# Kernel tuning notes

Measured on AMD Instinct MI355X. Metric: run time of the kernel, lower is better.

Reference implementation:

```python
import jax, jax.numpy as jnp
import numpy as np

N_NODES = 65536
N_EDGES = 1048576
IN_CH, HID_CH, OUT_CH = 300, 64, 20
DROPOUT_P = 0.5


def setup_inputs() -> dict:
    key = jax.random.key(0)
    ks = jax.random.split(key, 6)
    x = jax.random.normal(ks[0], (N_NODES, IN_CH), dtype=jnp.float32)
    edge_index = jax.random.randint(ks[1], (2, N_EDGES), 0, N_NODES, dtype=jnp.int64)
    edge_weight = jax.random.uniform(ks[2], (N_EDGES,), dtype=jnp.float32)
    # Glorot-ish init for linear weights (PyG lin has no bias; GCNConv adds its own bias)
    W1 = jax.random.normal(ks[3], (IN_CH, HID_CH), dtype=jnp.float32) / np.sqrt(IN_CH)
    b1 = jnp.zeros((HID_CH,), dtype=jnp.float32)
    W2 = jax.random.normal(ks[4], (HID_CH, OUT_CH), dtype=jnp.float32) / np.sqrt(HID_CH)
    b2 = jnp.zeros((OUT_CH,), dtype=jnp.float32)
    return {"x": x, "edge_index": edge_index, "edge_weight": edge_weight,
            "W1": W1, "b1": b1, "W2": W2, "b2": b2}


def _gcn_conv(x, src, dst, edge_weight, W, b, num_nodes):
    # GCNConv with add_self_loops=False, normalize=False:
    #   h = x @ W; out[i] = sum_{e: dst(e)=i} w_e * h[src(e)]; out += b
    h = x @ W                                   # [N, C_out]
    msg = h[src] * edge_weight[:, None]         # [E, C_out]
    agg = jax.ops.segment_sum(msg, dst, num_segments=num_nodes)
    return agg + b


def reference(x, edge_index, edge_weight, W1, b1, W2, b2):
    num_nodes = x.shape[0]
    src, dst = edge_index[0], edge_index[1]
    h = _gcn_conv(x, src, dst, edge_weight, W1, b1, num_nodes)
    h = jax.nn.relu(h)
    # dropout p=0.5, training=True, deterministic fixed key
    keep = jax.random.bernoulli(jax.random.key(42), 1.0 - DROPOUT_P, h.shape)
    h = jnp.where(keep, h / (1.0 - DROPOUT_P), 0.0)
    out = _gcn_conv(h, src, dst, edge_weight, W2, b2, num_nodes)
    return out
```

## Files before the change

kernel.cpp:

```cpp
#include <hip/hip_runtime.h>

#define N_NODES 65536
#define N_EDGES 1048576
#define NB 256
#define CAP 4608
#define EPB_A 4096
#define BLK_A (N_EDGES / EPB_A)
#define EPT_A (EPB_A / 1024)
#define WT_BLK 20
#define GEMM_BLK (N_NODES / 64)

typedef __attribute__((ext_vector_type(8))) short short8v;
typedef __attribute__((ext_vector_type(4))) float float4v;

__device__ __forceinline__ unsigned short f2bf(float f) {
  unsigned u = __float_as_uint(f);
  unsigned r = u + 0x7FFFu + ((u >> 16) & 1u);
  return (unsigned short)(r >> 16);
}
__device__ __forceinline__ float bflo(unsigned u) { return __uint_as_float(u << 16); }
__device__ __forceinline__ float bfhi(unsigned u) { return __uint_as_float(u & 0xFFFF0000u); }

__device__ __forceinline__ bool keep_mask(unsigned idx) {
  const unsigned k0 = 0u, k1 = 42u;
  const unsigned k2 = 0x1BD11BDAu ^ k0 ^ k1;
  unsigned x0 = 0u;
  unsigned x1 = idx;
  x0 += k0; x1 += k1;
#define TF_ROUND(r) { x0 += x1; x1 = (x1 << (r)) | (x1 >> (32 - (r))); x1 ^= x0; }
  TF_ROUND(13) TF_ROUND(15) TF_ROUND(26) TF_ROUND(6)
  x0 += k1; x1 += k2 + 1u;
  TF_ROUND(17) TF_ROUND(29) TF_ROUND(16) TF_ROUND(24)
  x0 += k2; x1 += k0 + 2u;
  TF_ROUND(13) TF_ROUND(15) TF_ROUND(26) TF_ROUND(6)
  x0 += k0; x1 += k1 + 3u;
  TF_ROUND(17) TF_ROUND(29) TF_ROUND(16) TF_ROUND(24)
  x0 += k1; x1 += k2 + 4u;
  TF_ROUND(13) TF_ROUND(15) TF_ROUND(26) TF_ROUND(6)
  x0 += k2; x1 += k0 + 5u;
#undef TF_ROUND
  return ((x0 ^ x1) & 0x80000000u) == 0u;
}

__global__ __launch_bounds__(1024) void binpass2(const int* __restrict__ ei,
                                                 const float* __restrict__ ew,
                                                 const float* __restrict__ W1,
                                                 unsigned* __restrict__ val2,
                                                 unsigned char* __restrict__ key2,
                                                 unsigned* __restrict__ cnt_mat,
                                                 unsigned* __restrict__ lofs_mat,
                                                 unsigned short* __restrict__ Wt) {
  const int b = blockIdx.x;
  const int t = threadIdx.x;
  if (b >= BLK_A) {
    int i = (b - BLK_A) * 1024 + t;
    int ch = i / 320, k = i % 320;
    Wt[i] = f2bf((k < 300) ? W1[k * 64 + ch] : 0.0f);
    return;
  }
  __shared__ unsigned cnt[NB], lofs[NB], lcur[NB];
  __shared__ unsigned stage_val[EPB_A];
  __shared__ unsigned char stage_key[EPB_A];
  const int e0 = b * EPB_A;
  if (t < NB) { cnt[t] = 0u; lcur[t] = 0u; }
  __syncthreads();
  unsigned pv[EPT_A], pb[EPT_A], pk8[EPT_A];
#pragma unroll
  for (int j = 0; j < EPT_A; ++j) {
    int e = e0 + t + j * 1024;
    unsigned s = (unsigned)ei[e];
    unsigned d = (unsigned)ei[N_EDGES + e];
    pv[j]  = s | ((unsigned)f2bf(ew[e]) << 16);
    pb[j]  = d >> 8;
    pk8[j] = d & 255u;
    atomicAdd(&cnt[pb[j]], 1u);
  }
  __syncthreads();
  if (t < NB) lofs[t] = cnt[t];
  __syncthreads();
  for (int d = 1; d < NB; d <<= 1) {
    unsigned u = 0u;
    if (t < NB && t >= d) u = lofs[t - d];
    __syncthreads();
    if (t < NB) lofs[t] += u;
    __syncthreads();
  }
  if (t < NB) {
    lofs[t] -= cnt[t];
    cnt_mat[(unsigned)b * NB + t]  = cnt[t];
    lofs_mat[(unsigned)b * NB + t] = lofs[t];
  }
  __syncthreads();
#pragma unroll
  for (int j = 0; j < EPT_A; ++j) {
    unsigned bk = pb[j];
    unsigned slot = lofs[bk] + atomicAdd(&lcur[bk], 1u);
    stage_val[slot] = pv[j];
    stage_key[slot] = (unsigned char)pk8[j];
  }
  __syncthreads();
  unsigned* dv = val2 + (size_t)b * EPB_A;
  unsigned char* dk = key2 + (size_t)b * EPB_A;
  for (int s = t; s < EPB_A; s += 1024) { dv[s] = stage_val[s]; dk[s] = stage_key[s]; }
}

__device__ __forceinline__ void bucket_body3(unsigned char* raw, int b,
                                             const unsigned* __restrict__ cnt_mat,
                                             const unsigned* __restrict__ lofs_mat,
                                             const unsigned* __restrict__ val2,
                                             const unsigned char* __restrict__ key2,
                                             unsigned* __restrict__ sortedc,
                                             unsigned* __restrict__ offs_p) {
  unsigned char* kLDS   = raw;
  unsigned* scnt_s  = (unsigned*)(raw + 4608);
  unsigned* sbase_s = scnt_s + NB;
  unsigned* mst_s   = sbase_s + NB;
  unsigned* cnt     = mst_s + NB;
  unsigned* cur     = cnt + NB;
  const int t = threadIdx.x;
  const unsigned scnt = cnt_mat[(unsigned)t * NB + b];
  const unsigned sofs = lofs_mat[(unsigned)t * NB + b];
  scnt_s[t]  = scnt;
  sbase_s[t] = (unsigned)t * EPB_A + sofs;
  cnt[t] = 0u;
  cur[t] = scnt;
  __syncthreads();
  for (int d = 1; d < NB; d <<= 1) {
    unsigned u = (t >= d) ? cur[t - d] : 0u;
    __syncthreads();
    cur[t] += u;
    __syncthreads();
  }
  mst_s[t] = cur[t] - scnt;
  __syncthreads();
  const unsigned n_edges = cur[NB - 1];
  const int g = t >> 4, j0 = t & 15;
  for (int seg = g; seg < NB; seg += 16) {
    const unsigned sc = scnt_s[seg];
    const unsigned sb = sbase_s[seg];
    const unsigned ms = mst_s[seg];
    for (unsigned j = (unsigned)j0; j < sc; j += 16)
      kLDS[ms + j] = key2[sb + j];
  }
  __syncthreads();
  for (unsigned i = t; i < n_edges; i += 256)
    atomicAdd(&cnt[kLDS[i]], 1u);
  __syncthreads();
  const unsigned myc = cnt[t];
  cur[t] = myc;
  __syncthreads();
  for (int d = 1; d < NB; d <<= 1) {
    unsigned u = (t >= d) ? cur[t - d] : 0u;
    __syncthreads();
    cur[t] += u;
    __syncthreads();
  }
  const unsigned lo = (unsigned)b * CAP;
  unsigned excl = cur[t] - myc;
  offs_p[b * NB + t] = (lo + excl) | (myc << 21);
  __syncthreads();
  cur[t] = excl;
  __syncthreads();
  for (int seg = g; seg < NB; seg += 16) {
    const unsigned sc = scnt_s[seg];
    const unsigned sb = sbase_s[seg];
    const unsigned ms = mst_s[seg];
    for (unsigned j = (unsigned)j0; j < sc; j += 16) {
      unsigned v = val2[sb + j];
      unsigned k = kLDS[ms + j];
      unsigned p = lo + atomicAdd(&cur[k], 1u);
      sortedc[p] = v;
    }
  }
}

__device__ __forceinline__ void gemm1_body(unsigned char* smraw, int nb,
                                           const float* __restrict__ x,
                                           const unsigned short* __restrict__ Wt,
                                           unsigned short* __restrict__ h1b) {
  unsigned short (*As)[72] = (unsigned short (*)[72])smraw;
  unsigned short (*Bs)[72] = (unsigned short (*)[72])(smraw + 9216);
  const int t = threadIdx.x;
  const int node0 = nb * 64;
  const int wave = t >> 6, lane = t & 63;
  const int quad = lane >> 4, l16 = lane & 15;
  float4v acc[4] = {{0.f,0.f,0.f,0.f},{0.f,0.f,0.f,0.f},{0.f,0.f,0.f,0.f},{0.f,0.f,0.f,0.f}};

  for (int kt = 0; kt < 5; ++kt) {
    const int k0 = kt * 64;
    for (int f = t; f < 1024; f += 256) {
      int node = f >> 4;
      int k = (f & 15) * 4;
      uint2 packed;
      if (k0 + k < 300) {
        float4 v = *(const float4*)(x + (size_t)(node0 + node) * 300 + k0 + k);
        packed.x = (unsigned)f2bf(v.x) | ((unsigned)f2bf(v.y) << 16);
        packed.y = (unsigned)f2bf(v.z) | ((unsigned)f2bf(v.w) << 16);
      } else {
        packed.x = 0u; packed.y = 0u;
      }
      *(uint2*)&As[node][k] = packed;
    }
    for (int f = t; f < 512; f += 256) {
      int ch = f >> 3;
      int kq = f & 7;
      uint4 v = *(const uint4*)(Wt + (size_t)ch * 320 + k0 + kq * 8);
      *(uint4*)&Bs[ch][kq * 8] = v;
    }
    __syncthreads();
    short8v a0 = *(const short8v*)&As[wave * 16 + l16][quad * 8];
    short8v a1 = *(const short8v*)&As[wave * 16 + l16][32 + quad * 8];
#pragma unroll
    for (int nt = 0; nt < 4; ++nt) {
      short8v b0 = *(const short8v*)&Bs[nt * 16 + l16][quad * 8];
      short8v b1 = *(const short8v*)&Bs[nt * 16 + l16][32 + quad * 8];
      acc[nt] = __builtin_amdgcn_mfma_f32_16x16x32_bf16(a0, b0, acc[nt], 0, 0, 0);
      acc[nt] = __builtin_amdgcn_mfma_f32_16x16x32_bf16(a1, b1, acc[nt], 0, 0, 0);
    }
    __syncthreads();
  }
#pragma unroll
  for (int nt = 0; nt < 4; ++nt) {
#pragma unroll
    for (int r = 0; r < 4; ++r) {
      h1b[(size_t)(node0 + wave * 16 + quad * 4 + r) * 64 + nt * 16 + l16] = f2bf(acc[nt][r]);
    }
  }
}

__global__ __launch_bounds__(256) void bucketsort_gemm1(const unsigned* __restrict__ cnt_mat,
                                                        const unsigned* __restrict__ lofs_mat,
                                                        const unsigned* __restrict__ val2,
                                                        const unsigned char* __restrict__ key2,
                                                        unsigned* __restrict__ sortedc,
                                                        unsigned* __restrict__ offs_p,
                                                        const float* __restrict__ x,
                                                        const unsigned short* __restrict__ Wt,
                                                        unsigned short* __restrict__ h1b) {
  __shared__ __align__(16) unsigned char sm[18432];
  if (blockIdx.x < NB) {
    bucket_body3(sm, blockIdx.x, cnt_mat, lofs_mat, val2, key2, sortedc, offs_p);
  } else {
    gemm1_body(sm, blockIdx.x - NB, x, Wt, h1b);
  }
}

__global__ __launch_bounds__(256) void agg1_gemm2(const unsigned* __restrict__ offs_p,
                                                  const unsigned* __restrict__ sortedc,
                                                  const unsigned short* __restrict__ h1b,
                                                  const float* __restrict__ b1,
                                                  const float* __restrict__ W2,
                                                  unsigned* __restrict__ g32u) {
  __shared__ float h2[16][68];
  __shared__ float w2t[20][68];
  const int t = threadIdx.x;
  const int node0 = blockIdx.x * 16;
  for (int i = t; i < 20 * 64; i += 256) {
    int row = i >> 6, col = i & 63;
    w2t[row][col] = W2[col * 20 + row];
  }
  const int n = t >> 4, cg = t & 15;
  const int node = node0 + n;
  const unsigned op = offs_p[node];
  const unsigned s = op & 0x1FFFFFu;
  const unsigned e_end = s + (op >> 21);
  float4 acc = *(const float4*)(b1 + cg * 4);
  unsigned i = s;
  for (; i + 8 <= e_end; i += 8) {
    unsigned e0 = sortedc[i],     e1 = sortedc[i + 1], e2 = sortedc[i + 2], e3 = sortedc[i + 3];
    unsigned e4 = sortedc[i + 4], e5 = sortedc[i + 5], e6 = sortedc[i + 6], e7 = sortedc[i + 7];
    uint2 v0 = *(const uint2*)(h1b + ((size_t)(e0 & 0xFFFFu)) * 64 + cg * 4);
    uint2 v1 = *(const uint2*)(h1b + ((size_t)(e1 & 0xFFFFu)) * 64 + cg * 4);
    uint2 v2 = *(const uint2*)(h1b + ((size_t)(e2 & 0xFFFFu)) * 64 + cg * 4);
    uint2 v3 = *(const uint2*)(h1b + ((size_t)(e3 & 0xFFFFu)) * 64 + cg * 4);
    uint2 v4 = *(const uint2*)(h1b + ((size_t)(e4 & 0xFFFFu)) * 64 + cg * 4);
    uint2 v5 = *(const uint2*)(h1b + ((size_t)(e5 & 0xFFFFu)) * 64 + cg * 4);
    uint2 v6 = *(const uint2*)(h1b + ((size_t)(e6 & 0xFFFFu)) * 64 + cg * 4);
    uint2 v7 = *(const uint2*)(h1b + ((size_t)(e7 & 0xFFFFu)) * 64 + cg * 4);
    float w0 = bfhi(e0), w1 = bfhi(e1), w2 = bfhi(e2), w3 = bfhi(e3);
    float w4 = bfhi(e4), w5 = bfhi(e5), w6 = bfhi(e6), w7 = bfhi(e7);
    acc.x = fmaf(w0, bflo(v0.x), acc.x); acc.y = fmaf(w0, bfhi(v0.x), acc.y);
    acc.z = fmaf(w0, bflo(v0.y), acc.z); acc.w = fmaf(w0, bfhi(v0.y), acc.w);
    acc.x = fmaf(w1, bflo(v1.x), acc.x); acc.y = fmaf(w1, bfhi(v1.x), acc.y);
    acc.z = fmaf(w1, bflo(v1.y), acc.z); acc.w = fmaf(w1, bfhi(v1.y), acc.w);
    acc.x = fmaf(w2, bflo(v2.x), acc.x); acc.y = fmaf(w2, bfhi(v2.x), acc.y);
    acc.z = fmaf(w2, bflo(v2.y), acc.z); acc.w = fmaf(w2, bfhi(v2.y), acc.w);
    acc.x = fmaf(w3, bflo(v3.x), acc.x); acc.y = fmaf(w3, bfhi(v3.x), acc.y);
    acc.z = fmaf(w3, bflo(v3.y), acc.z); acc.w = fmaf(w3, bfhi(v3.y), acc.w);
    acc.x = fmaf(w4, bflo(v4.x), acc.x); acc.y = fmaf(w4, bfhi(v4.x), acc.y);
    acc.z = fmaf(w4, bflo(v4.y), acc.z); acc.w = fmaf(w4, bfhi(v4.y), acc.w);
    acc.x = fmaf(w5, bflo(v5.x), acc.x); acc.y = fmaf(w5, bfhi(v5.x), acc.y);
    acc.z = fmaf(w5, bflo(v5.y), acc.z); acc.w = fmaf(w5, bfhi(v5.y), acc.w);
    acc.x = fmaf(w6, bflo(v6.x), acc.x); acc.y = fmaf(w6, bfhi(v6.x), acc.y);
    acc.z = fmaf(w6, bflo(v6.y), acc.z); acc.w = fmaf(w6, bfhi(v6.y), acc.w);
    acc.x = fmaf(w7, bflo(v7.x), acc.x); acc.y = fmaf(w7, bfhi(v7.x), acc.y);
    acc.z = fmaf(w7, bflo(v7.y), acc.z); acc.w = fmaf(w7, bfhi(v7.y), acc.w);
  }
  for (; i < e_end; ++i) {
    unsigned e0 = sortedc[i];
    uint2 v0 = *(const uint2*)(h1b + ((size_t)(e0 & 0xFFFFu)) * 64 + cg * 4);
    float w0 = bfhi(e0);
    acc.x = fmaf(w0, bflo(v0.x), acc.x); acc.y = fmaf(w0, bfhi(v0.x), acc.y);
    acc.z = fmaf(w0, bflo(v0.y), acc.z); acc.w = fmaf(w0, bfhi(v0.y), acc.w);
  }
  const unsigned gi = (unsigned)node * 64u + (unsigned)cg * 4u;
  float r[4] = {acc.x, acc.y, acc.z, acc.w};
#pragma unroll
  for (int j = 0; j < 4; ++j) {
    float v = fmaxf(r[j], 0.0f);
    h2[n][cg * 4 + j] = keep_mask(gi + j) ? v * 2.0f : 0.0f;
  }
  __syncthreads();
  float d0 = 0.0f, d1 = 0.0f;
  if (cg < 10) {
    const int c0 = cg * 2, c1 = cg * 2 + 1;
#pragma unroll
    for (int k = 0; k < 64; k += 4) {
      float4 hv = *(const float4*)(&h2[n][k]);
      float4 w0 = *(const float4*)(&w2t[c0][k]);
      float4 w1 = *(const float4*)(&w2t[c1][k]);
      d0 = fmaf(hv.x, w0.x, d0); d0 = fmaf(hv.y, w0.y, d0);
      d0 = fmaf(hv.z, w0.z, d0); d0 = fmaf(hv.w, w0.w, d0);
      d1 = fmaf(hv.x, w1.x, d1); d1 = fmaf(hv.y, w1.y, d1);
      d1 = fmaf(hv.z, w1.z, d1); d1 = fmaf(hv.w, w1.w, d1);
    }
  }
  unsigned packed = (cg < 10) ? ((unsigned)f2bf(d0) | ((unsigned)f2bf(d1) << 16)) : 0u;
  g32u[(size_t)node * 16 + cg] = packed;
}

__global__ __launch_bounds__(256) void aggregate2(const unsigned* __restrict__ offs_p,
                                                  const unsigned* __restrict__ sortedc,
                                                  const unsigned* __restrict__ g32u,
                                                  const float* __restrict__ b2,
                                                  float* __restrict__ out) {
  const int t = threadIdx.x;
  const int n = blockIdx.x * 16 + (t >> 4);
  const int cg = t & 15;
  const unsigned op = offs_p[n];
  const unsigned s = op & 0x1FFFFFu;
  const unsigned e_end = s + (op >> 21);
  float ax = 0.0f, ay = 0.0f;
  unsigned i = s;
  for (; i + 8 <= e_end; i += 8) {
    unsigned e0 = sortedc[i],     e1 = sortedc[i + 1], e2 = sortedc[i + 2], e3 = sortedc[i + 3];
    unsigned e4 = sortedc[i + 4], e5 = sortedc[i + 5], e6 = sortedc[i + 6], e7 = sortedc[i + 7];
    unsigned v0 = g32u[(size_t)(e0 & 0xFFFFu) * 16 + cg];
    unsigned v1 = g32u[(size_t)(e1 & 0xFFFFu) * 16 + cg];
    unsigned v2 = g32u[(size_t)(e2 & 0xFFFFu) * 16 + cg];
    unsigned v3 = g32u[(size_t)(e3 & 0xFFFFu) * 16 + cg];
    unsigned v4 = g32u[(size_t)(e4 & 0xFFFFu) * 16 + cg];
    unsigned v5 = g32u[(size_t)(e5 & 0xFFFFu) * 16 + cg];
    unsigned v6 = g32u[(size_t)(e6 & 0xFFFFu) * 16 + cg];
    unsigned v7 = g32u[(size_t)(e7 & 0xFFFFu) * 16 + cg];
    float w0 = bfhi(e0), w1 = bfhi(e1), w2 = bfhi(e2), w3 = bfhi(e3);
    float w4 = bfhi(e4), w5 = bfhi(e5), w6 = bfhi(e6), w7 = bfhi(e7);
    ax = fmaf(w0, bflo(v0), ax); ay = fmaf(w0, bfhi(v0), ay);
    ax = fmaf(w1, bflo(v1), ax); ay = fmaf(w1, bfhi(v1), ay);
    ax = fmaf(w2, bflo(v2), ax); ay = fmaf(w2, bfhi(v2), ay);
    ax = fmaf(w3, bflo(v3), ax); ay = fmaf(w3, bfhi(v3), ay);
    ax = fmaf(w4, bflo(v4), ax); ay = fmaf(w4, bfhi(v4), ay);
    ax = fmaf(w5, bflo(v5), ax); ay = fmaf(w5, bfhi(v5), ay);
    ax = fmaf(w6, bflo(v6), ax); ay = fmaf(w6, bfhi(v6), ay);
    ax = fmaf(w7, bflo(v7), ax); ay = fmaf(w7, bfhi(v7), ay);
  }
  for (; i < e_end; ++i) {
    unsigned e0 = sortedc[i];
    unsigned v0 = g32u[(size_t)(e0 & 0xFFFFu) * 16 + cg];
    float w0 = bfhi(e0);
    ax = fmaf(w0, bflo(v0), ax); ay = fmaf(w0, bfhi(v0), ay);
  }
  if (cg < 10) {
    float2 o = make_float2(ax + b2[cg * 2], ay + b2[cg * 2 + 1]);
    *(float2*)(out + (size_t)n * 20 + cg * 2) = o;
  }
}

extern "C" void kernel_launch(void* const* d_in, const int* in_sizes, int n_in,
                              void* d_out, int out_size, void* d_ws, size_t ws_size,
                              hipStream_t stream) {
  const float* x  = (const float*)d_in[0];
  const int*   ei = (const int*)d_in[1];
  const float* ew = (const float*)d_in[2];
  const float* W1 = (const float*)d_in[3];
  const float* b1 = (const float*)d_in[4];
  const float* W2 = (const float*)d_in[5];
  const float* b2 = (const float*)d_in[6];
  float* out = (float*)d_out;

  unsigned short* h1b      = (unsigned short*)d_ws;
  unsigned*       g32u     = (unsigned*)(h1b + (size_t)N_NODES * 64);
  unsigned*       val2     = g32u + (size_t)N_NODES * 16;
  unsigned*       sortedc  = val2 + (size_t)N_EDGES;
  unsigned*       offs_p   = sortedc + (size_t)NB * CAP;
  unsigned*       cnt_mat  = offs_p + N_NODES;
  unsigned*       lofs_mat = cnt_mat + (size_t)BLK_A * NB;
  unsigned char*  key2     = (unsigned char*)(lofs_mat + (size_t)BLK_A * NB);
  unsigned short* Wt       = (unsigned short*)(key2 + (size_t)N_EDGES);

  binpass2<<<BLK_A + WT_BLK, 1024, 0, stream>>>(ei, ew, W1, val2, key2, cnt_mat, lofs_mat, Wt);
  bucketsort_gemm1<<<NB + GEMM_BLK, 256, 0, stream>>>(cnt_mat, lofs_mat, val2, key2,
                                                      sortedc, offs_p, x, Wt, h1b);
  agg1_gemm2<<<N_NODES / 16, 256, 0, stream>>>(offs_p, sortedc, h1b, b1, W2, g32u);
  aggregate2<<<N_NODES / 16, 256, 0, stream>>>(offs_p, sortedc, g32u, b2, out);
}
```

Before: 212.2 us.

## Restructure pipeline: fuse binning with GEMM1 and bucket sort with layer-1 aggregation

```diff
diff --git a/kernel.cpp b/kernel.cpp
--- a/kernel.cpp
+++ b/kernel.cpp
@@ -6,8 +6,7 @@
 #define CAP 4608
 #define EPB_A 4096
 #define BLK_A (N_EDGES / EPB_A)
-#define EPT_A (EPB_A / 1024)
-#define WT_BLK 20
+#define EPT_A (EPB_A / 256)
 #define GEMM_BLK (N_NODES / 64)
 
 typedef __attribute__((ext_vector_type(8))) short short8v;
@@ -42,141 +41,62 @@
   return ((x0 ^ x1) & 0x80000000u) == 0u;
 }
 
-__global__ __launch_bounds__(1024) void binpass2(const int* __restrict__ ei,
-                                                 const float* __restrict__ ew,
-                                                 const float* __restrict__ W1,
-                                                 unsigned* __restrict__ val2,
-                                                 unsigned char* __restrict__ key2,
-                                                 unsigned* __restrict__ cnt_mat,
-                                                 unsigned* __restrict__ lofs_mat,
-                                                 unsigned short* __restrict__ Wt) {
-  const int b = blockIdx.x;
+__device__ __forceinline__ void binpass_body(unsigned char* raw, int b,
+                                             const int* __restrict__ ei,
+                                             const float* __restrict__ ew,
+                                             unsigned* __restrict__ val2,
+                                             unsigned char* __restrict__ key2,
+                                             unsigned* __restrict__ cnt_mat,
+                                             unsigned* __restrict__ lofs_mat) {
+  unsigned* stage_val      = (unsigned*)raw;
+  unsigned char* stage_key = raw + 16384;
+  unsigned* cnt  = (unsigned*)(raw + 20480);
+  unsigned* lofs = cnt + NB;
+  unsigned* lcur = lofs + NB;
   const int t = threadIdx.x;
-  if (b >= BLK_A) {
-    int i = (b - BLK_A) * 1024 + t;
-    int ch = i / 320, k = i % 320;
-    Wt[i] = f2bf((k < 300) ? W1[k * 64 + ch] : 0.0f);
-    return;
-  }
-  __shared__ unsigned cnt[NB], lofs[NB], lcur[NB];
-  __shared__ unsigned stage_val[EPB_A];
-  __shared__ unsigned char stage_key[EPB_A];
   const int e0 = b * EPB_A;
-  if (t < NB) { cnt[t] = 0u; lcur[t] = 0u; }
-  __syncthreads();
-  unsigned pv[EPT_A], pb[EPT_A], pk8[EPT_A];
+  cnt[t] = 0u;
+  lcur[t] = 0u;
+  __syncthreads();
+  unsigned pv[EPT_A], pd[EPT_A];
 #pragma unroll
   for (int j = 0; j < EPT_A; ++j) {
-    int e = e0 + t + j * 1024;
+    int e = e0 + t + j * 256;
     unsigned s = (unsigned)ei[e];
     unsigned d = (unsigned)ei[N_EDGES + e];
-    pv[j]  = s | ((unsigned)f2bf(ew[e]) << 16);
-    pb[j]  = d >> 8;
-    pk8[j] = d & 255u;
-    atomicAdd(&cnt[pb[j]], 1u);
-  }
-  __syncthreads();
-  if (t < NB) lofs[t] = cnt[t];
+    pv[j] = s | ((unsigned)f2bf(ew[e]) << 16);
+    pd[j] = d;
+    atomicAdd(&cnt[d >> 8], 1u);
+  }
+  __syncthreads();
+  lofs[t] = cnt[t];
   __syncthreads();
   for (int d = 1; d < NB; d <<= 1) {
-    unsigned u = 0u;
-    if (t < NB && t >= d) u = lofs[t - d];
-    __syncthreads();
-    if (t < NB) lofs[t] += u;
-    __syncthreads();
-  }
-  if (t < NB) {
-    lofs[t] -= cnt[t];
-    cnt_mat[(unsigned)b * NB + t]  = cnt[t];
-    lofs_mat[(unsigned)b * NB + t] = lofs[t];
-  }
+    unsigned u = (t >= d) ? lofs[t - d] : 0u;
+    __syncthreads();
+    lofs[t] += u;
+    __syncthreads();
+  }
+  lofs[t] -= cnt[t];
+  cnt_mat[(unsigned)b * NB + t]  = cnt[t];
+  lofs_mat[(unsigned)b * NB + t] = lofs[t];
   __syncthreads();
 #pragma unroll
   for (int j = 0; j < EPT_A; ++j) {
-    unsigned bk = pb[j];
+    unsigned bk = pd[j] >> 8;
     unsigned slot = lofs[bk] + atomicAdd(&lcur[bk], 1u);
     stage_val[slot] = pv[j];
-    stage_key[slot] = (unsigned char)pk8[j];
+    stage_key[slot] = (unsigned char)(pd[j] & 255u);
   }
   __syncthreads();
   unsigned* dv = val2 + (size_t)b * EPB_A;
   unsigned char* dk = key2 + (size_t)b * EPB_A;
-  for (int s = t; s < EPB_A; s += 1024) { dv[s] = stage_val[s]; dk[s] = stage_key[s]; }
-}
-
-__device__ __forceinline__ void bucket_body3(unsigned char* raw, int b,
-                                             const unsigned* __restrict__ cnt_mat,
-                                             const unsigned* __restrict__ lofs_mat,
-                                             const unsigned* __restrict__ val2,
-                                             const unsigned char* __restrict__ key2,
-                                             unsigned* __restrict__ sortedc,
-                                             unsigned* __restrict__ offs_p) {
-  unsigned char* kLDS   = raw;
-  unsigned* scnt_s  = (unsigned*)(raw + 4608);
-  unsigned* sbase_s = scnt_s + NB;
-  unsigned* mst_s   = sbase_s + NB;
-  unsigned* cnt     = mst_s + NB;
-  unsigned* cur     = cnt + NB;
-  const int t = threadIdx.x;
-  const unsigned scnt = cnt_mat[(unsigned)t * NB + b];
-  const unsigned sofs = lofs_mat[(unsigned)t * NB + b];
-  scnt_s[t]  = scnt;
-  sbase_s[t] = (unsigned)t * EPB_A + sofs;
-  cnt[t] = 0u;
-  cur[t] = scnt;
-  __syncthreads();
-  for (int d = 1; d < NB; d <<= 1) {
-    unsigned u = (t >= d) ? cur[t - d] : 0u;
-    __syncthreads();
-    cur[t] += u;
-    __syncthreads();
-  }
-  mst_s[t] = cur[t] - scnt;
-  __syncthreads();
-  const unsigned n_edges = cur[NB - 1];
-  const int g = t >> 4, j0 = t & 15;
-  for (int seg = g; seg < NB; seg += 16) {
-    const unsigned sc = scnt_s[seg];
-    const unsigned sb = sbase_s[seg];
-    const unsigned ms = mst_s[seg];
-    for (unsigned j = (unsigned)j0; j < sc; j += 16)
-      kLDS[ms + j] = key2[sb + j];
-  }
-  __syncthreads();
-  for (unsigned i = t; i < n_edges; i += 256)
-    atomicAdd(&cnt[kLDS[i]], 1u);
-  __syncthreads();
-  const unsigned myc = cnt[t];
-  cur[t] = myc;
-  __syncthreads();
-  for (int d = 1; d < NB; d <<= 1) {
-    unsigned u = (t >= d) ? cur[t - d] : 0u;
-    __syncthreads();
-    cur[t] += u;
-    __syncthreads();
-  }
-  const unsigned lo = (unsigned)b * CAP;
-  unsigned excl = cur[t] - myc;
-  offs_p[b * NB + t] = (lo + excl) | (myc << 21);
-  __syncthreads();
-  cur[t] = excl;
-  __syncthreads();
-  for (int seg = g; seg < NB; seg += 16) {
-    const unsigned sc = scnt_s[seg];
-    const unsigned sb = sbase_s[seg];
-    const unsigned ms = mst_s[seg];
-    for (unsigned j = (unsigned)j0; j < sc; j += 16) {
-      unsigned v = val2[sb + j];
-      unsigned k = kLDS[ms + j];
-      unsigned p = lo + atomicAdd(&cur[k], 1u);
-      sortedc[p] = v;
-    }
-  }
+  for (int s = t; s < EPB_A; s += 256) { dv[s] = stage_val[s]; dk[s] = stage_key[s]; }
 }
 
 __device__ __forceinline__ void gemm1_body(unsigned char* smraw, int nb,
                                            const float* __restrict__ x,
-                                           const unsigned short* __restrict__ Wt,
+                                           const float* __restrict__ W1,
                                            unsigned short* __restrict__ h1b) {
   unsigned short (*As)[72] = (unsigned short (*)[72])smraw;
   unsigned short (*Bs)[72] = (unsigned short (*)[72])(smraw + 9216);
@@ -204,7 +124,17 @@
     for (int f = t; f < 512; f += 256) {
       int ch = f >> 3;
       int kq = f & 7;
-      uint4 v = *(const uint4*)(Wt + (size_t)ch * 320 + k0 + kq * 8);
+      unsigned short tmp[8];
+#pragma unroll
+      for (int m = 0; m < 8; ++m) {
+        int k = k0 + kq * 8 + m;
+        tmp[m] = (k < 300) ? f2bf(W1[(size_t)k * 64 + ch]) : (unsigned short)0;
+      }
+      uint4 v;
+      v.x = (unsigned)tmp[0] | ((unsigned)tmp[1] << 16);
+      v.y = (unsigned)tmp[2] | ((unsigned)tmp[3] << 16);
+      v.z = (unsigned)tmp[4] | ((unsigned)tmp[5] << 16);
+      v.w = (unsigned)tmp[6] | ((unsigned)tmp[7] << 16);
       *(uint4*)&Bs[ch][kq * 8] = v;
     }
     __syncthreads();
@@ -228,105 +158,181 @@
   }
 }
 
-__global__ __launch_bounds__(256) void bucketsort_gemm1(const unsigned* __restrict__ cnt_mat,
-                                                        const unsigned* __restrict__ lofs_mat,
-                                                        const unsigned* __restrict__ val2,
-                                                        const unsigned char* __restrict__ key2,
-                                                        unsigned* __restrict__ sortedc,
-                                                        unsigned* __restrict__ offs_p,
-                                                        const float* __restrict__ x,
-                                                        const unsigned short* __restrict__ Wt,
-                                                        unsigned short* __restrict__ h1b) {
-  __shared__ __align__(16) unsigned char sm[18432];
-  if (blockIdx.x < NB) {
-    bucket_body3(sm, blockIdx.x, cnt_mat, lofs_mat, val2, key2, sortedc, offs_p);
+__global__ __launch_bounds__(256) void binpass_gemm1(const int* __restrict__ ei,
+                                                     const float* __restrict__ ew,
+                                                     unsigned* __restrict__ val2,
+                                                     unsigned char* __restrict__ key2,
+                                                     unsigned* __restrict__ cnt_mat,
+                                                     unsigned* __restrict__ lofs_mat,
+                                                     const float* __restrict__ x,
+                                                     const float* __restrict__ W1,
+                                                     unsigned short* __restrict__ h1b) {
+  __shared__ __align__(16) unsigned char sm[23552];
+  if (blockIdx.x < BLK_A) {
+    binpass_body(sm, blockIdx.x, ei, ew, val2, key2, cnt_mat, lofs_mat);
   } else {
-    gemm1_body(sm, blockIdx.x - NB, x, Wt, h1b);
-  }
-}
-
-__global__ __launch_bounds__(256) void agg1_gemm2(const unsigned* __restrict__ offs_p,
-                                                  const unsigned* __restrict__ sortedc,
-                                                  const unsigned short* __restrict__ h1b,
-                                                  const float* __restrict__ b1,
-                                                  const float* __restrict__ W2,
-                                                  unsigned* __restrict__ g32u) {
-  __shared__ float h2[16][68];
-  __shared__ float w2t[20][68];
+    gemm1_body(sm, blockIdx.x - BLK_A, x, W1, h1b);
+  }
+}
+
+__global__ __launch_bounds__(1024) void sortagg1(const unsigned* __restrict__ cnt_mat,
+                                                 const unsigned* __restrict__ lofs_mat,
+                                                 const unsigned* __restrict__ val2,
+                                                 const unsigned char* __restrict__ key2,
+                                                 unsigned* __restrict__ sortedc,
+                                                 unsigned* __restrict__ offs_p,
+                                                 const unsigned short* __restrict__ h1b,
+                                                 const float* __restrict__ b1,
+                                                 const float* __restrict__ W2,
+                                                 unsigned* __restrict__ g32u) {
+  __shared__ __align__(16) unsigned char raw[54080];
+  unsigned*      uval   = (unsigned*)raw;
+  unsigned char* ukey   = raw + 18432;
+  unsigned*      sval   = (unsigned*)(raw + 23040);
+  unsigned* scnt_s  = (unsigned*)(raw + 41472);
+  unsigned* sbase_s = scnt_s + NB;
+  unsigned* mst_s   = sbase_s + NB;
+  unsigned* cnt     = mst_s + NB;
+  unsigned* cur     = cnt + NB;
+  unsigned* stn     = cur + NB;
+  unsigned* ctn     = stn + NB;
+  float*    h2      = (float*)raw;
+  float*    w2t     = (float*)(raw + 48640);
   const int t = threadIdx.x;
-  const int node0 = blockIdx.x * 16;
-  for (int i = t; i < 20 * 64; i += 256) {
+  const int b = blockIdx.x;
+  const unsigned lo = (unsigned)b * CAP;
+
+  for (int i = t; i < 20 * 64; i += 1024) {
     int row = i >> 6, col = i & 63;
-    w2t[row][col] = W2[col * 20 + row];
-  }
+    w2t[row * 68 + col] = W2[col * 20 + row];
+  }
+  if (t < NB) {
+    unsigned sc = cnt_mat[(unsigned)t * NB + b];
+    scnt_s[t]  = sc;
+    sbase_s[t] = (unsigned)t * EPB_A + lofs_mat[(unsigned)t * NB + b];
+    cnt[t] = 0u;
+    cur[t] = sc;
+  }
+  __syncthreads();
+  for (int d = 1; d < NB; d <<= 1) {
+    unsigned u = (t < NB && t >= d) ? cur[t - d] : 0u;
+    __syncthreads();
+    if (t < NB) cur[t] += u;
+    __syncthreads();
+  }
+  if (t < NB) mst_s[t] = cur[t] - scnt_s[t];
+  __syncthreads();
+  const unsigned n_edges = cur[NB - 1];
+  const int g = t >> 4, j0 = t & 15;
+  for (int seg = g; seg < NB; seg += 64) {
+    const unsigned sc = scnt_s[seg];
+    const unsigned sb = sbase_s[seg];
+    const unsigned ms = mst_s[seg];
+    for (unsigned j = (unsigned)j0; j < sc; j += 16) {
+      uval[ms + j] = val2[sb + j];
+      ukey[ms + j] = key2[sb + j];
+    }
+  }
+  __syncthreads();
+  for (unsigned i = t; i < n_edges; i += 1024)
+    atomicAdd(&cnt[ukey[i]], 1u);
+  __syncthreads();
+  if (t < NB) cur[t] = cnt[t];
+  __syncthreads();
+  for (int d = 1; d < NB; d <<= 1) {
+    unsigned u = (t < NB && t >= d) ? cur[t - d] : 0u;
+    __syncthreads();
+    if (t < NB) cur[t] += u;
+    __syncthreads();
+  }
+  if (t < NB) {
+    unsigned excl = cur[t] - cnt[t];
+    stn[t] = excl;
+    ctn[t] = cnt[t];
+    offs_p[b * NB + t] = (lo + excl) | (cnt[t] << 21);
+    cur[t] = excl;
+  }
+  __syncthreads();
+  for (unsigned i = t; i < n_edges; i += 1024) {
+    unsigned k = ukey[i];
+    unsigned p = atomicAdd(&cur[k], 1u);
+    sval[p] = uval[i];
+  }
+  __syncthreads();
+  for (unsigned i = t; i < n_edges; i += 1024) sortedc[lo + i] = sval[i];
+  __syncthreads();
+
   const int n = t >> 4, cg = t & 15;
-  const int node = node0 + n;
-  const unsigned op = offs_p[node];
-  const unsigned s = op & 0x1FFFFFu;
-  const unsigned e_end = s + (op >> 21);
-  float4 acc = *(const float4*)(b1 + cg * 4);
-  unsigned i = s;
-  for (; i + 8 <= e_end; i += 8) {
-    unsigned e0 = sortedc[i],     e1 = sortedc[i + 1], e2 = sortedc[i + 2], e3 = sortedc[i + 3];
-    unsigned e4 = sortedc[i + 4], e5 = sortedc[i + 5], e6 = sortedc[i + 6], e7 = sortedc[i + 7];
-    uint2 v0 = *(const uint2*)(h1b + ((size_t)(e0 & 0xFFFFu)) * 64 + cg * 4);
-    uint2 v1 = *(const uint2*)(h1b + ((size_t)(e1 & 0xFFFFu)) * 64 + cg * 4);
-    uint2 v2 = *(const uint2*)(h1b + ((size_t)(e2 & 0xFFFFu)) * 64 + cg * 4);
-    uint2 v3 = *(const uint2*)(h1b + ((size_t)(e3 & 0xFFFFu)) * 64 + cg * 4);
-    uint2 v4 = *(const uint2*)(h1b + ((size_t)(e4 & 0xFFFFu)) * 64 + cg * 4);
-    uint2 v5 = *(const uint2*)(h1b + ((size_t)(e5 & 0xFFFFu)) * 64 + cg * 4);
-    uint2 v6 = *(const uint2*)(h1b + ((size_t)(e6 & 0xFFFFu)) * 64 + cg * 4);
-    uint2 v7 = *(const uint2*)(h1b + ((size_t)(e7 & 0xFFFFu)) * 64 + cg * 4);
-    float w0 = bfhi(e0), w1 = bfhi(e1), w2 = bfhi(e2), w3 = bfhi(e3);
-    float w4 = bfhi(e4), w5 = bfhi(e5), w6 = bfhi(e6), w7 = bfhi(e7);
-    acc.x = fmaf(w0, bflo(v0.x), acc.x); acc.y = fmaf(w0, bfhi(v0.x), acc.y);
-    acc.z = fmaf(w0, bflo(v0.y), acc.z); acc.w = fmaf(w0, bfhi(v0.y), acc.w);
-    acc.x = fmaf(w1, bflo(v1.x), acc.x); acc.y = fmaf(w1, bfhi(v1.x), acc.y);
-    acc.z = fmaf(w1, bflo(v1.y), acc.z); acc.w = fmaf(w1, bfhi(v1.y), acc.w);
-    acc.x = fmaf(w2, bflo(v2.x), acc.x); acc.y = fmaf(w2, bfhi(v2.x), acc.y);
-    acc.z = fmaf(w2, bflo(v2.y), acc.z); acc.w = fmaf(w2, bfhi(v2.y), acc.w);
-    acc.x = fmaf(w3, bflo(v3.x), acc.x); acc.y = fmaf(w3, bfhi(v3.x), acc.y);
-    acc.z = fmaf(w3, bflo(v3.y), acc.z); acc.w = fmaf(w3, bfhi(v3.y), acc.w);
-    acc.x = fmaf(w4, bflo(v4.x), acc.x); acc.y = fmaf(w4, bfhi(v4.x), acc.y);
-    acc.z = fmaf(w4, bflo(v4.y), acc.z); acc.w = fmaf(w4, bfhi(v4.y), acc.w);
-    acc.x = fmaf(w5, bflo(v5.x), acc.x); acc.y = fmaf(w5, bfhi(v5.x), acc.y);
-    acc.z = fmaf(w5, bflo(v5.y), acc.z); acc.w = fmaf(w5, bfhi(v5.y), acc.w);
-    acc.x = fmaf(w6, bflo(v6.x), acc.x); acc.y = fmaf(w6, bfhi(v6.x), acc.y);
-    acc.z = fmaf(w6, bflo(v6.y), acc.z); acc.w = fmaf(w6, bfhi(v6.y), acc.w);
-    acc.x = fmaf(w7, bflo(v7.x), acc.x); acc.y = fmaf(w7, bfhi(v7.x), acc.y);
-    acc.z = fmaf(w7, bflo(v7.y), acc.z); acc.w = fmaf(w7, bfhi(v7.y), acc.w);
-  }
-  for (; i < e_end; ++i) {
-    unsigned e0 = sortedc[i];
-    uint2 v0 = *(const uint2*)(h1b + ((size_t)(e0 & 0xFFFFu)) * 64 + cg * 4);
-    float w0 = bfhi(e0);
-    acc.x = fmaf(w0, bflo(v0.x), acc.x); acc.y = fmaf(w0, bfhi(v0.x), acc.y);
-    acc.z = fmaf(w0, bflo(v0.y), acc.z); acc.w = fmaf(w0, bfhi(v0.y), acc.w);
-  }
-  const unsigned gi = (unsigned)node * 64u + (unsigned)cg * 4u;
-  float r[4] = {acc.x, acc.y, acc.z, acc.w};
-#pragma unroll
-  for (int j = 0; j < 4; ++j) {
-    float v = fmaxf(r[j], 0.0f);
-    h2[n][cg * 4 + j] = keep_mask(gi + j) ? v * 2.0f : 0.0f;
-  }
-  __syncthreads();
-  float d0 = 0.0f, d1 = 0.0f;
-  if (cg < 10) {
-    const int c0 = cg * 2, c1 = cg * 2 + 1;
-#pragma unroll
-    for (int k = 0; k < 64; k += 4) {
-      float4 hv = *(const float4*)(&h2[n][k]);
-      float4 w0 = *(const float4*)(&w2t[c0][k]);
-      float4 w1 = *(const float4*)(&w2t[c1][k]);
-      d0 = fmaf(hv.x, w0.x, d0); d0 = fmaf(hv.y, w0.y, d0);
-      d0 = fmaf(hv.z, w0.z, d0); d0 = fmaf(hv.w, w0.w, d0);
-      d1 = fmaf(hv.x, w1.x, d1); d1 = fmaf(hv.y, w1.y, d1);
-      d1 = fmaf(hv.z, w1.z, d1); d1 = fmaf(hv.w, w1.w, d1);
-    }
-  }
-  unsigned packed = (cg < 10) ? ((unsigned)f2bf(d0) | ((unsigned)f2bf(d1) << 16)) : 0u;
-  g32u[(size_t)node * 16 + cg] = packed;
+  for (int chunk = 0; chunk < 4; ++chunk) {
+    const int ln = chunk * 64 + n;
+    const unsigned node = (unsigned)b * 256u + (unsigned)ln;
+    const unsigned s = stn[ln];
+    const unsigned e_end = s + ctn[ln];
+    float4 acc = *(const float4*)(b1 + cg * 4);
+    unsigned i = s;
+    for (; i + 8 <= e_end; i += 8) {
+      unsigned e0 = sval[i],     e1 = sval[i + 1], e2 = sval[i + 2], e3 = sval[i + 3];
+      unsigned e4 = sval[i + 4], e5 = sval[i + 5], e6 = sval[i + 6], e7 = sval[i + 7];
+      uint2 v0 = *(const uint2*)(h1b + ((size_t)(e0 & 0xFFFFu)) * 64 + cg * 4);
+      uint2 v1 = *(const uint2*)(h1b + ((size_t)(e1 & 0xFFFFu)) * 64 + cg * 4);
+      uint2 v2 = *(const uint2*)(h1b + ((size_t)(e2 & 0xFFFFu)) * 64 + cg * 4);
+      uint2 v3 = *(const uint2*)(h1b + ((size_t)(e3 & 0xFFFFu)) * 64 + cg * 4);
+      uint2 v4 = *(const uint2*)(h1b + ((size_t)(e4 & 0xFFFFu)) * 64 + cg * 4);
+      uint2 v5 = *(const uint2*)(h1b + ((size_t)(e5 & 0xFFFFu)) * 64 + cg * 4);
+      uint2 v6 = *(const uint2*)(h1b + ((size_t)(e6 & 0xFFFFu)) * 64 + cg * 4);
+      uint2 v7 = *(const uint2*)(h1b + ((size_t)(e7 & 0xFFFFu)) * 64 + cg * 4);
+      float w0 = bfhi(e0), w1 = bfhi(e1), w2 = bfhi(e2), w3 = bfhi(e3);
+      float w4 = bfhi(e4), w5 = bfhi(e5), w6 = bfhi(e6), w7 = bfhi(e7);
+      acc.x = fmaf(w0, bflo(v0.x), acc.x); acc.y = fmaf(w0, bfhi(v0.x), acc.y);
+      acc.z = fmaf(w0, bflo(v0.y), acc.z); acc.w = fmaf(w0, bfhi(v0.y), acc.w);
+      acc.x = fmaf(w1, bflo(v1.x), acc.x); acc.y = fmaf(w1, bfhi(v1.x), acc.y);
+      acc.z = fmaf(w1, bflo(v1.y), acc.z); acc.w = fmaf(w1, bfhi(v1.y), acc.w);
+      acc.x = fmaf(w2, bflo(v2.x), acc.x); acc.y = fmaf(w2, bfhi(v2.x), acc.y);
+      acc.z = fmaf(w2, bflo(v2.y), acc.z); acc.w = fmaf(w2, bfhi(v2.y), acc.w);
+      acc.x = fmaf(w3, bflo(v3.x), acc.x); acc.y = fmaf(w3, bfhi(v3.x), acc.y);
+      acc.z = fmaf(w3, bflo(v3.y), acc.z); acc.w = fmaf(w3, bfhi(v3.y), acc.w);
+      acc.x = fmaf(w4, bflo(v4.x), acc.x); acc.y = fmaf(w4, bfhi(v4.x), acc.y);
+      acc.z = fmaf(w4, bflo(v4.y), acc.z); acc.w = fmaf(w4, bfhi(v4.y), acc.w);
+      acc.x = fmaf(w5, bflo(v5.x), acc.x); acc.y = fmaf(w5, bfhi(v5.x), acc.y);
+      acc.z = fmaf(w5, bflo(v5.y), acc.z); acc.w = fmaf(w5, bfhi(v5.y), acc.w);
+      acc.x = fmaf(w6, bflo(v6.x), acc.x); acc.y = fmaf(w6, bfhi(v6.x), acc.y);
+      acc.z = fmaf(w6, bflo(v6.y), acc.z); acc.w = fmaf(w6, bfhi(v6.y), acc.w);
+      acc.x = fmaf(w7, bflo(v7.x), acc.x); acc.y = fmaf(w7, bfhi(v7.x), acc.y);
+      acc.z = fmaf(w7, bflo(v7.y), acc.z); acc.w = fmaf(w7, bfhi(v7.y), acc.w);
+    }
+    for (; i < e_end; ++i) {
+      unsigned e0 = sval[i];
+      uint2 v0 = *(const uint2*)(h1b + ((size_t)(e0 & 0xFFFFu)) * 64 + cg * 4);
+      float w0 = bfhi(e0);
+      acc.x = fmaf(w0, bflo(v0.x), acc.x); acc.y = fmaf(w0, bfhi(v0.x), acc.y);
+      acc.z = fmaf(w0, bflo(v0.y), acc.z); acc.w = fmaf(w0, bfhi(v0.y), acc.w);
+    }
+    const unsigned gi = node * 64u + (unsigned)cg * 4u;
+    float r[4] = {acc.x, acc.y, acc.z, acc.w};
+#pragma unroll
+    for (int j = 0; j < 4; ++j) {
+      float v = fmaxf(r[j], 0.0f);
+      h2[n * 68 + cg * 4 + j] = keep_mask(gi + j) ? v * 2.0f : 0.0f;
+    }
+    __syncthreads();
+    float d0 = 0.0f, d1 = 0.0f;
+    if (cg < 10) {
+      const int c0 = cg * 2, c1 = cg * 2 + 1;
+#pragma unroll
+      for (int k = 0; k < 64; k += 4) {
+        float4 hv = *(const float4*)(&h2[n * 68 + k]);
+        float4 w0 = *(const float4*)(&w2t[c0 * 68 + k]);
+        float4 w1 = *(const float4*)(&w2t[c1 * 68 + k]);
+        d0 = fmaf(hv.x, w0.x, d0); d0 = fmaf(hv.y, w0.y, d0);
+        d0 = fmaf(hv.z, w0.z, d0); d0 = fmaf(hv.w, w0.w, d0);
+        d1 = fmaf(hv.x, w1.x, d1); d1 = fmaf(hv.y, w1.y, d1);
+        d1 = fmaf(hv.z, w1.z, d1); d1 = fmaf(hv.w, w1.w, d1);
+      }
+    }
+    unsigned packed = (cg < 10) ? ((unsigned)f2bf(d0) | ((unsigned)f2bf(d1) << 16)) : 0u;
+    g32u[(size_t)node * 16 + cg] = packed;
+    __syncthreads();
+  }
 }
 
 __global__ __launch_bounds__(256) void aggregate2(const unsigned* __restrict__ offs_p,
@@ -396,11 +402,10 @@
   unsigned*       cnt_mat  = offs_p + N_NODES;
   unsigned*       lofs_mat = cnt_mat + (size_t)BLK_A * NB;
   unsigned char*  key2     = (unsigned char*)(lofs_mat + (size_t)BLK_A * NB);
-  unsigned short* Wt       = (unsigned short*)(key2 + (size_t)N_EDGES);
-
-  binpass2<<<BLK_A + WT_BLK, 1024, 0, stream>>>(ei, ew, W1, val2, key2, cnt_mat, lofs_mat, Wt);
-  bucketsort_gemm1<<<NB + GEMM_BLK, 256, 0, stream>>>(cnt_mat, lofs_mat, val2, key2,
-                                                      sortedc, offs_p, x, Wt, h1b);
-  agg1_gemm2<<<N_NODES / 16, 256, 0, stream>>>(offs_p, sortedc, h1b, b1, W2, g32u);
+
+  binpass_gemm1<<<BLK_A + GEMM_BLK, 256, 0, stream>>>(ei, ew, val2, key2, cnt_mat,
+                                                      lofs_mat, x, W1, h1b);
+  sortagg1<<<NB, 1024, 0, stream>>>(cnt_mat, lofs_mat, val2, key2, sortedc, offs_p,
+                                    h1b, b1, W2, g32u);
   aggregate2<<<N_NODES / 16, 256, 0, stream>>>(offs_p, sortedc, g32u, b2, out);
 }
```

Measured after the change: 242.1 us. 1.14x slower.
